# Kernel tuning notes

Measured on AMD Instinct MI355X. Metric: run time of the kernel, lower is better.

Reference implementation:

```python
import jax, jax.numpy as jnp
import numpy as np
from jax import lax

NUM_MARKETS = 32
WINDOW = 16
T = 1048576


def setup_inputs() -> dict:
    key = jax.random.key(0)
    k1, k2, k3, k4 = jax.random.split(key, 4)
    std = float(np.sqrt(WINDOW))  # matches nn.init.normal_(.., 0, sqrt(window_size))
    x = jax.random.normal(k1, (1, NUM_MARKETS, T), dtype=jnp.float32)
    start_pos = -jnp.ones((NUM_MARKETS, 1), dtype=jnp.float32)  # default start_pos = -1
    conv_w = jax.random.normal(k2, (NUM_MARKETS, NUM_MARKETS, WINDOW), dtype=jnp.float32) * std
    conv_b = jax.random.normal(k3, (NUM_MARKETS,), dtype=jnp.float32) * 0.05
    pos_weight = jax.random.normal(k4, (NUM_MARKETS, 1), dtype=jnp.float32) * std
    return {"x": x, "start_pos": start_pos, "conv_w": conv_w, "conv_b": conv_b, "pos_weight": pos_weight}


def reference(x, start_pos, conv_w, conv_b, pos_weight):
    # Conv1d, valid padding: [1, N, T] -> [1, N, L], L = T - WINDOW + 1
    y = lax.conv_general_dilated(
        x, conv_w, window_strides=(1,), padding="VALID",
        dimension_numbers=("NCH", "OIH", "NCH"),
    ) + conv_b[None, :, None]
    seq = y[0].T  # [L, N] time-major for the scan
    pw = pos_weight[:, 0]  # [N]

    def step(pos, xt):
        a = jnp.tanh(pos * pw + xt)  # [N]
        return jnp.sign(a), a

    _, outs = lax.scan(step, start_pos[:, 0], seq)  # outs: [L, N]
    positions = jnp.concatenate([start_pos, outs.T], axis=1)  # [N, L+1]
    return positions[None]  # [1, N, L+1]
```

## Files before the change

### kernel.cpp

```cpp
#include <hip/hip_runtime.h>
#include <stdint.h>

#define T_LEN    1048576
#define TY_LEN   1048561
#define OUT_W    1048562
#define NM       32
#define WIN      16
#define NCH      4096
#define CL       256
#define CBT      256
#define TPB      256
#define XS_W     272
#define NF4      68

__device__ inline float sgnf(float a){
    return (a > 0.0f) ? 1.0f : ((a < 0.0f) ? -1.0f : 0.0f);
}

__global__ void wtrans_kernel(const float* __restrict__ w, float* __restrict__ wT2){
    const int idx = blockIdx.x * 256 + threadIdx.x;
    if (idx >= NM * NM * WIN) return;
    const int o = idx / (NM * WIN);
    const int r = idx - o * (NM * WIN);
    const int i = r / WIN;
    const int h = r - i * WIN;
    wT2[(((h * 4) + (o >> 3)) * NM + i) * 8 + (o & 7)] = w[idx];
}

__global__ __launch_bounds__(256, 4) void conv_kernel(
    const float* __restrict__ x, const float* __restrict__ wT2,
    const float* __restrict__ b, float* __restrict__ out)
{
    __shared__ float xs[NM * XS_W];
    const int base = blockIdx.x * TPB;
    for (int idx = threadIdx.x; idx < NM * NF4; idx += CBT) {
        const int i = idx / NF4;
        const int q = idx - i * NF4;
        const int t0 = base + q * 4;
        float4 v;
        if (t0 + 3 < T_LEN) {
            v = *reinterpret_cast<const float4*>(x + (size_t)i * T_LEN + t0);
        } else {
            v.x = (t0 + 0 < T_LEN) ? x[(size_t)i * T_LEN + t0 + 0] : 0.0f;
            v.y = (t0 + 1 < T_LEN) ? x[(size_t)i * T_LEN + t0 + 1] : 0.0f;
            v.z = (t0 + 2 < T_LEN) ? x[(size_t)i * T_LEN + t0 + 2] : 0.0f;
            v.w = (t0 + 3 < T_LEN) ? x[(size_t)i * T_LEN + t0 + 3] : 0.0f;
        }
        *reinterpret_cast<float4*>(&xs[i * XS_W + q * 4]) = v;
    }
    __syncthreads();
    const int lane = threadIdx.x & 63;
    const int og   = __builtin_amdgcn_readfirstlane(threadIdx.x >> 6);
    float acc[8][4];
#pragma unroll
    for (int oi = 0; oi < 8; ++oi)
#pragma unroll
        for (int tt = 0; tt < 4; ++tt) acc[oi][tt] = 0.0f;
#pragma unroll 1
    for (int h = 0; h < WIN; ++h) {
        const float* wp = wT2 + (size_t)(h * 4 + og) * (NM * 8);
#pragma unroll 1
        for (int c = 0; c < 4; ++c) {
            float xv[8][4];
#pragma unroll
            for (int i2 = 0; i2 < 8; ++i2) {
                const int i = c * 8 + i2;
#pragma unroll
                for (int tt = 0; tt < 4; ++tt)
                    xv[i2][tt] = xs[i * XS_W + lane + 64 * tt + h];
            }
#pragma unroll
            for (int i2 = 0; i2 < 8; ++i2) {
                const float* wr = wp + (c * 8 + i2) * 8;
#pragma unroll
                for (int oi = 0; oi < 8; ++oi) {
                    const float wv = wr[oi];
#pragma unroll
                    for (int tt = 0; tt < 4; ++tt)
                        acc[oi][tt] = fmaf(wv, xv[i2][tt], acc[oi][tt]);
                }
            }
        }
    }
#pragma unroll
    for (int oi = 0; oi < 8; ++oi) {
        const int o = og * 8 + oi;
        const float bv = b[o];
        float* orow = out + (size_t)o * OUT_W + 1 + base + lane;
#pragma unroll
        for (int tt = 0; tt < 4; ++tt) {
            const int t = base + lane + 64 * tt;
            if (t < TY_LEN) orow[64 * tt] = acc[oi][tt] + bv;
        }
    }
}

__global__ __launch_bounds__(256) void scan_pass_a(
    const float* __restrict__ yb, const float* __restrict__ sp,
    const float* __restrict__ pwv, uint32_t* __restrict__ trans)
{
    const int gid = blockIdx.x * 256 + threadIdx.x;
    const int m = gid >> 12;
    const int c = gid & (NCH - 1);
    const float pw = pwv[m];
    float p0 = -1.0f, p1 = 0.0f, p2 = 1.0f, p3 = sp[m];
    const float* hr = yb + (size_t)m * OUT_W + 1 + c * CL;
    const int limit0 = TY_LEN - c * CL;
    const int limit = limit0 < CL ? limit0 : CL;
    int j = 0;
    for (; j + 4 <= limit; j += 4) {
        const float4 h = *reinterpret_cast<const float4*>(hr + j);
#define STEPA(hv) { const float hv_ = (hv); \
        p0 = sgnf(fmaf(p0, pw, hv_)); \
        p1 = sgnf(fmaf(p1, pw, hv_)); \
        p2 = sgnf(fmaf(p2, pw, hv_)); \
        p3 = sgnf(fmaf(p3, pw, hv_)); }
        STEPA(h.x); STEPA(h.y); STEPA(h.z); STEPA(h.w);
    }
    for (; j < limit; ++j) { STEPA(hr[j]); }
#undef STEPA
    const uint32_t e0 = (uint32_t)((int)p0 + 1);
    const uint32_t e1 = (uint32_t)((int)p1 + 1);
    const uint32_t e2 = (uint32_t)((int)p2 + 1);
    const uint32_t e3 = (uint32_t)((int)p3 + 1);
    trans[m * NCH + c] = e0 | (e1 << 8) | (e2 << 16) | (e3 << 24);
}

__device__ inline uint32_t map_comp(uint32_t f, uint32_t g){
    uint32_t r = 0;
#pragma unroll
    for (int k = 0; k < 4; ++k) {
        const uint32_t s = (g >> (8 * k)) & 0xFFu;
        const uint32_t o = (f >> (8 * s)) & 0xFFu;
        r |= o << (8 * k);
    }
    return r;
}

__global__ __launch_bounds__(256) void scan_pass_b(
    const uint32_t* __restrict__ trans, uint8_t* __restrict__ entries)
{
    const uint32_t ID = 0x03020100u;
    const int m = blockIdx.x;
    const int tid = threadIdx.x;
    __shared__ uint32_t S[256];
    uint32_t maps[16];
    uint32_t seg = ID;
    const uint32_t* tr = trans + m * NCH + tid * 16;
#pragma unroll
    for (int j = 0; j < 16; ++j) { maps[j] = tr[j]; seg = map_comp(maps[j], seg); }
    S[tid] = seg;
    __syncthreads();
    for (int off = 1; off < 256; off <<= 1) {
        const uint32_t v = (tid >= off) ? S[tid - off] : ID;
        __syncthreads();
        if (tid >= off) S[tid] = map_comp(S[tid], v);
        __syncthreads();
    }
    const uint32_t pre = (tid == 0) ? ID : S[tid - 1];
    uint32_t s = (pre >> 24) & 0xFFu;
    uint8_t* er = entries + m * NCH + tid * 16;
#pragma unroll
    for (int j = 0; j < 16; ++j) {
        er[j] = (uint8_t)s;
        s = (maps[j] >> (8 * s)) & 0xFFu;
    }
}

__global__ __launch_bounds__(256) void scan_pass_c(
    float* yo, const float* __restrict__ sp, const float* __restrict__ pwv,
    const uint8_t* __restrict__ entries)
{
    const int gid = blockIdx.x * 256 + threadIdx.x;
    const int m = gid >> 12;
    const int c = gid & (NCH - 1);
    const float pw = pwv[m];
    const float spv = sp[m];
    const uint32_t s = entries[m * NCH + c];
    float p = (s == 3u) ? spv : ((float)(int)s - 1.0f);
    float* row = yo + (size_t)m * OUT_W + 1 + c * CL;
    if (c == 0) yo[(size_t)m * OUT_W] = spv;
    const int limit0 = TY_LEN - c * CL;
    const int limit = limit0 < CL ? limit0 : CL;
    int j = 0;
    for (; j + 4 <= limit; j += 4) {
        const float4 h = *reinterpret_cast<const float4*>(row + j);
        float a;
        a = fmaf(p, pw, h.x); row[j+0] = tanhf(a); p = sgnf(a);
        a = fmaf(p, pw, h.y); row[j+1] = tanhf(a); p = sgnf(a);
        a = fmaf(p, pw, h.z); row[j+2] = tanhf(a); p = sgnf(a);
        a = fmaf(p, pw, h.w); row[j+3] = tanhf(a); p = sgnf(a);
    }
    for (; j < limit; ++j) {
        const float a = fmaf(p, pw, row[j]);
        row[j] = tanhf(a);
        p = sgnf(a);
    }
}

extern "C" void kernel_launch(void* const* d_in, const int* in_sizes, int n_in,
                              void* d_out, int out_size, void* d_ws, size_t ws_size,
                              hipStream_t stream)
{
    const float* x   = (const float*)d_in[0];
    const float* spv = (const float*)d_in[1];
    const float* w   = (const float*)d_in[2];
    const float* b   = (const float*)d_in[3];
    const float* pw  = (const float*)d_in[4];
    float* out = (float*)d_out;

    uint8_t* ws = (uint8_t*)d_ws;
    float*    wT2     = (float*)ws;
    uint32_t* trans   = (uint32_t*)(ws + 65536);
    uint8_t*  entries = (uint8_t*)(ws + 65536 + 524288);

    const int conv_blocks = (TY_LEN + TPB - 1) / TPB;
    wtrans_kernel<<<64, 256, 0, stream>>>(w, wT2);
    conv_kernel<<<conv_blocks, CBT, 0, stream>>>(x, wT2, b, out);
    scan_pass_a<<<(NM * NCH) / 256, 256, 0, stream>>>(out, spv, pw, trans);
    scan_pass_b<<<NM, 256, 0, stream>>>(trans, entries);
    scan_pass_c<<<(NM * NCH) / 256, 256, 0, stream>>>(out, spv, pw, entries);
}
```

Baseline: 522.8 us.

## Fuse scan pass A into conv kernel via shared-memory staging of outputs

The conv kernel now stages its biased outputs in shared memory. The first 32 threads then compute each market's per-chunk sign-transition map from those values and write it to trans. This removes the separate scan_pass_a launch and its full re-read of the conv output from global memory. The cost is an extra barrier and a serial 256-step loop run by only 32 threads per block, which lengthens each conv block's tail.

```diff
diff --git a/kernel.cpp b/kernel.cpp
--- a/kernel.cpp
+++ b/kernel.cpp
@@ -12,6 +12,7 @@
 #define TPB      256
 #define XS_W     272
 #define NF4      68
+#define YS_W     257
 
 __device__ inline float sgnf(float a){
     return (a > 0.0f) ? 1.0f : ((a < 0.0f) ? -1.0f : 0.0f);
@@ -29,7 +30,9 @@
 
 __global__ __launch_bounds__(256, 4) void conv_kernel(
     const float* __restrict__ x, const float* __restrict__ wT2,
-    const float* __restrict__ b, float* __restrict__ out)
+    const float* __restrict__ b, const float* __restrict__ sp,
+    const float* __restrict__ pwv, float* __restrict__ out,
+    uint32_t* __restrict__ trans)
 {
     __shared__ float xs[NM * XS_W];
     const int base = blockIdx.x * TPB;
@@ -82,48 +85,49 @@
             }
         }
     }
+    float yv[8][4];
+    __syncthreads();
 #pragma unroll
     for (int oi = 0; oi < 8; ++oi) {
         const int o = og * 8 + oi;
         const float bv = b[o];
+#pragma unroll
+        for (int tt = 0; tt < 4; ++tt) {
+            yv[oi][tt] = acc[oi][tt] + bv;
+            xs[o * YS_W + lane + 64 * tt] = yv[oi][tt];
+        }
+    }
+    __syncthreads();
+#pragma unroll
+    for (int oi = 0; oi < 8; ++oi) {
+        const int o = og * 8 + oi;
         float* orow = out + (size_t)o * OUT_W + 1 + base + lane;
 #pragma unroll
         for (int tt = 0; tt < 4; ++tt) {
             const int t = base + lane + 64 * tt;
-            if (t < TY_LEN) orow[64 * tt] = acc[oi][tt] + bv;
-        }
-    }
-}
-
-__global__ __launch_bounds__(256) void scan_pass_a(
-    const float* __restrict__ yb, const float* __restrict__ sp,
-    const float* __restrict__ pwv, uint32_t* __restrict__ trans)
-{
-    const int gid = blockIdx.x * 256 + threadIdx.x;
-    const int m = gid >> 12;
-    const int c = gid & (NCH - 1);
-    const float pw = pwv[m];
-    float p0 = -1.0f, p1 = 0.0f, p2 = 1.0f, p3 = sp[m];
-    const float* hr = yb + (size_t)m * OUT_W + 1 + c * CL;
-    const int limit0 = TY_LEN - c * CL;
-    const int limit = limit0 < CL ? limit0 : CL;
-    int j = 0;
-    for (; j + 4 <= limit; j += 4) {
-        const float4 h = *reinterpret_cast<const float4*>(hr + j);
-#define STEPA(hv) { const float hv_ = (hv); \
-        p0 = sgnf(fmaf(p0, pw, hv_)); \
-        p1 = sgnf(fmaf(p1, pw, hv_)); \
-        p2 = sgnf(fmaf(p2, pw, hv_)); \
-        p3 = sgnf(fmaf(p3, pw, hv_)); }
-        STEPA(h.x); STEPA(h.y); STEPA(h.z); STEPA(h.w);
-    }
-    for (; j < limit; ++j) { STEPA(hr[j]); }
-#undef STEPA
-    const uint32_t e0 = (uint32_t)((int)p0 + 1);
-    const uint32_t e1 = (uint32_t)((int)p1 + 1);
-    const uint32_t e2 = (uint32_t)((int)p2 + 1);
-    const uint32_t e3 = (uint32_t)((int)p3 + 1);
-    trans[m * NCH + c] = e0 | (e1 << 8) | (e2 << 16) | (e3 << 24);
+            if (t < TY_LEN) orow[64 * tt] = yv[oi][tt];
+        }
+    }
+    if (threadIdx.x < NM) {
+        const int m = threadIdx.x;
+        const float pw = pwv[m];
+        float p0 = -1.0f, p1 = 0.0f, p2 = 1.0f, p3 = sp[m];
+        const int rem = TY_LEN - base;
+        const int limit = rem < TPB ? rem : TPB;
+        const float* yr = &xs[m * YS_W];
+        for (int j = 0; j < limit; ++j) {
+            const float hv = yr[j];
+            p0 = sgnf(fmaf(p0, pw, hv));
+            p1 = sgnf(fmaf(p1, pw, hv));
+            p2 = sgnf(fmaf(p2, pw, hv));
+            p3 = sgnf(fmaf(p3, pw, hv));
+        }
+        const uint32_t e0 = (uint32_t)((int)p0 + 1);
+        const uint32_t e1 = (uint32_t)((int)p1 + 1);
+        const uint32_t e2 = (uint32_t)((int)p2 + 1);
+        const uint32_t e3 = (uint32_t)((int)p3 + 1);
+        trans[m * NCH + blockIdx.x] = e0 | (e1 << 8) | (e2 << 16) | (e3 << 24);
+    }
 }
 
 __device__ inline uint32_t map_comp(uint32_t f, uint32_t g){
@@ -214,10 +218,9 @@
     uint32_t* trans   = (uint32_t*)(ws + 65536);
     uint8_t*  entries = (uint8_t*)(ws + 65536 + 524288);
 
-    const int conv_blocks = (TY_LEN + TPB - 1) / TPB;
+    const int conv_blocks = NCH;
     wtrans_kernel<<<64, 256, 0, stream>>>(w, wT2);
-    conv_kernel<<<conv_blocks, CBT, 0, stream>>>(x, wT2, b, out);
-    scan_pass_a<<<(NM * NCH) / 256, 256, 0, stream>>>(out, spv, pw, trans);
+    conv_kernel<<<conv_blocks, CBT, 0, stream>>>(x, wT2, b, spv, pw, out, trans);
     scan_pass_b<<<NM, 256, 0, stream>>>(trans, entries);
     scan_pass_c<<<(NM * NCH) / 256, 256, 0, stream>>>(out, spv, pw, entries);
 }
```

Measured after the change: 537.9 us. +2.9%, slower.
